# Kernel tuning notes

Measured on AMD Instinct MI355X. Metric: run time of the kernel, lower is better.

Reference implementation:

```python
import jax, jax.numpy as jnp
import numpy as np

N_NODES = 100000
N_GRAPHS = 512


def gcn_conv(x, W, b, src, dst, n_nodes):
    """PyG GCNConv: out = D^{-1/2} (A + I) D^{-1/2} (x W) + b, scatter at dst."""
    xw = x @ W  # [N, out_dim]
    # add self loops
    loop = jnp.arange(n_nodes, dtype=src.dtype)
    src_f = jnp.concatenate([src, loop])
    dst_f = jnp.concatenate([dst, loop])
    # symmetric normalization: deg from unit edge weights on dst
    deg = jax.ops.segment_sum(jnp.ones_like(dst_f, dtype=xw.dtype), dst_f,
                              num_segments=n_nodes)
    dinv = jnp.where(deg > 0, jax.lax.rsqrt(deg), 0.0)
    norm = dinv[src_f] * dinv[dst_f]  # [E+N]
    msg = xw[src_f] * norm[:, None]   # gather + scale, [E+N, out_dim]
    out = jax.ops.segment_sum(msg, dst_f, num_segments=n_nodes)
    return out + b


def global_mean_pool(x, batch, num_graphs):
    s = jax.ops.segment_sum(x, batch, num_segments=num_graphs)
    cnt = jax.ops.segment_sum(jnp.ones((x.shape[0],), x.dtype), batch,
                              num_segments=num_graphs)
    return s / jnp.maximum(cnt, 1.0)[:, None]


def setup_inputs() -> dict:
    key = jax.random.key(0)
    ks = jax.random.split(key, 10)
    d_in, h1, h2, d_out = 128, 128, 128, 32
    n_edges = 1600000
    x = jax.random.normal(ks[0], (N_NODES, d_in), dtype=jnp.float32)
    edge_index = jax.random.randint(ks[1], (2, n_edges), 0, N_NODES, dtype=jnp.int64)
    batch = jnp.sort(jax.random.randint(ks[2], (N_NODES,), 0, N_GRAPHS, dtype=jnp.int64))
    s1 = 1.0 / np.sqrt(d_in)
    s2 = 1.0 / np.sqrt(h1)
    s3 = 1.0 / np.sqrt(h2)
    W1 = jax.random.uniform(ks[3], (d_in, h1), jnp.float32, -s1, s1)
    b1 = jnp.zeros((h1,), jnp.float32)
    W2 = jax.random.uniform(ks[4], (h1, h2), jnp.float32, -s2, s2)
    b2 = jnp.zeros((h2,), jnp.float32)
    Wl = jax.random.uniform(ks[5], (h2, d_out), jnp.float32, -s3 * np.sqrt(6.0), s3 * np.sqrt(6.0))
    bl = jax.random.uniform(ks[6], (d_out,), jnp.float32, -s3, s3)
    return {"x": x, "edge_index": edge_index, "batch": batch,
            "W1": W1, "b1": b1, "W2": W2, "b2": b2, "Wl": Wl, "bl": bl}


def reference(x, edge_index, batch, W1, b1, W2, b2, Wl, bl):
    src, dst = edge_index[0], edge_index[1]
    h = gcn_conv(x, W1, b1, src, dst, N_NODES)
    h = jax.nn.relu(h)
    h = gcn_conv(h, W2, b2, src, dst, N_NODES)
    g = global_mean_pool(h, batch, N_GRAPHS)
    g = jax.nn.relu(g)
    return g @ Wl + bl
```

## Files before the change

### kernel.cpp

```cpp
#include <hip/hip_runtime.h>
#include <hip/hip_fp16.h>

#define DIM 128
#define NGRAPH 512
#define BUCKET_SHIFT 9
#define BUCKET_NODES 512

typedef _Float16 half8 __attribute__((ext_vector_type(8)));
typedef float floatx4 __attribute__((ext_vector_type(4)));

__device__ __forceinline__ int detect64(const int* __restrict__ ei) {
  int all0 = 1;
#pragma unroll
  for (int k = 0; k < 32; ++k) all0 &= (ei[2 * k + 1] == 0);
  return all0;
}

__device__ __forceinline__ int edge_at(const int* p, long long idx, int is64) {
  return is64 ? p[idx * 2] : p[(size_t)idx];
}

__global__ __launch_bounds__(256) void k_bucket_hist(const int* __restrict__ ei, int E,
                                                     int* __restrict__ bucket_count,
                                                     int nbuck) {
  __shared__ int h[256];
  int tid = threadIdx.x;
  h[tid] = 0;
  __syncthreads();
  int is64 = detect64(ei);
  int half = E >> 1;
  if (is64) {
    const int4* dp = (const int4*)(ei + 2 * (size_t)E);
    for (int t = blockIdx.x * 256 + tid; t < half; t += gridDim.x * 256) {
      int4 d = dp[t];
      atomicAdd(&h[d.x >> BUCKET_SHIFT], 1);
      atomicAdd(&h[d.z >> BUCKET_SHIFT], 1);
    }
  } else {
    const int2* dp = (const int2*)(ei + (size_t)E);
    for (int t = blockIdx.x * 256 + tid; t < half; t += gridDim.x * 256) {
      int2 d = dp[t];
      atomicAdd(&h[d.x >> BUCKET_SHIFT], 1);
      atomicAdd(&h[d.y >> BUCKET_SHIFT], 1);
    }
  }
  __syncthreads();
  if (tid < nbuck && h[tid]) atomicAdd(&bucket_count[tid], h[tid]);
  if ((E & 1) && blockIdx.x == 0 && tid == 0) {
    int d = edge_at(ei, (long long)E + (E - 1), is64);
    atomicAdd(&bucket_count[d >> BUCKET_SHIFT], 1);
  }
}

__global__ __launch_bounds__(256) void k_bucket_scan(const int* __restrict__ bucket_count,
                                                     int* __restrict__ bucket_off,
                                                     int* __restrict__ bucket_cursor,
                                                     int* __restrict__ row_off,
                                                     int nbuck, int N, int E) {
  __shared__ int s[256];
  int t = threadIdx.x;
  int v = (t < nbuck) ? bucket_count[t] : 0;
  s[t] = v;
  __syncthreads();
  for (int off = 1; off < 256; off <<= 1) {
    int u = (t >= off) ? s[t - off] : 0;
    __syncthreads();
    s[t] += u;
    __syncthreads();
  }
  int excl = s[t] - v;
  if (t < nbuck) { bucket_off[t] = excl; bucket_cursor[t] = excl; }
  if (t == 0) { bucket_off[nbuck] = E; row_off[N] = E; }
}

__global__ __launch_bounds__(256) void k_scatter(const int* __restrict__ ei, int E,
                                                 int* __restrict__ flag,
                                                 int* __restrict__ bucket_cursor,
                                                 int2* __restrict__ staging, int nbuck) {
  __shared__ int h[256];
  __shared__ int basebuf[256];
  int tid = threadIdx.x;
  int half = E >> 1;
  int ppb = (half + gridDim.x - 1) / gridDim.x;
  int lo = blockIdx.x * ppb;
  int hi = min(lo + ppb, half);
  h[tid] = 0;
  __syncthreads();
  int is64 = detect64(ei);
  if (blockIdx.x == 0 && tid == 0) *flag = is64;
  if (is64) {
    const int4* dp = (const int4*)(ei + 2 * (size_t)E);
    for (int t = lo + tid; t < hi; t += 256) {
      int4 d = dp[t];
      atomicAdd(&h[d.x >> BUCKET_SHIFT], 1);
      atomicAdd(&h[d.z >> BUCKET_SHIFT], 1);
    }
  } else {
    const int2* dp = (const int2*)(ei + (size_t)E);
    for (int t = lo + tid; t < hi; t += 256) {
      int2 d = dp[t];
      atomicAdd(&h[d.x >> BUCKET_SHIFT], 1);
      atomicAdd(&h[d.y >> BUCKET_SHIFT], 1);
    }
  }
  __syncthreads();
  if (tid < nbuck) {
    int c = h[tid];
    if (c) basebuf[tid] = atomicAdd(&bucket_cursor[tid], c);
    h[tid] = 0;
  }
  __syncthreads();
  if (is64) {
    const int4* sp = (const int4*)ei;
    const int4* dp = (const int4*)(ei + 2 * (size_t)E);
    for (int t = lo + tid; t < hi; t += 256) {
      int4 sv = sp[t];
      int4 dv = dp[t];
      int b0 = dv.x >> BUCKET_SHIFT;
      int l0 = atomicAdd(&h[b0], 1);
      staging[basebuf[b0] + l0] = make_int2(sv.x, dv.x);
      int b1 = dv.z >> BUCKET_SHIFT;
      int l1 = atomicAdd(&h[b1], 1);
      staging[basebuf[b1] + l1] = make_int2(sv.z, dv.z);
    }
  } else {
    const int2* sp = (const int2*)ei;
    const int2* dp = (const int2*)(ei + (size_t)E);
    for (int t = lo + tid; t < hi; t += 256) {
      int2 sv = sp[t];
      int2 dv = dp[t];
      int b0 = dv.x >> BUCKET_SHIFT;
      int l0 = atomicAdd(&h[b0], 1);
      staging[basebuf[b0] + l0] = make_int2(sv.x, dv.x);
      int b1 = dv.y >> BUCKET_SHIFT;
      int l1 = atomicAdd(&h[b1], 1);
      staging[basebuf[b1] + l1] = make_int2(sv.y, dv.y);
    }
  }
  if ((E & 1) && blockIdx.x == 0 && tid == 0) {
    int s0 = edge_at(ei, E - 1, is64);
    int d0 = edge_at(ei, (long long)E + (E - 1), is64);
    int pos = atomicAdd(&bucket_cursor[d0 >> BUCKET_SHIFT], 1);
    staging[pos] = make_int2(s0, d0);
  }
}

__global__ __launch_bounds__(256) void k_csr_build(const int2* __restrict__ staging,
                                                   const int* __restrict__ bucket_off,
                                                   int* __restrict__ row_off,
                                                   float* __restrict__ dinv,
                                                   int* __restrict__ csr_src, int N) {
  __shared__ int cnt_s[BUCKET_NODES];
  __shared__ int s[256];
  int tid = threadIdx.x;
  int b = blockIdx.x;
  int base = b << BUCKET_SHIFT;
  cnt_s[tid] = 0;
  cnt_s[tid + 256] = 0;
  __syncthreads();
  int start = bucket_off[b], end = bucket_off[b + 1];
  for (int i = start + tid; i < end; i += 256) {
    int2 e = staging[i];
    atomicAdd(&cnt_s[e.y - base], 1);
  }
  __syncthreads();
  int a0 = cnt_s[2 * tid], a1 = cnt_s[2 * tid + 1];
  int ps = a0 + a1;
  s[tid] = ps;
  __syncthreads();
  for (int off = 1; off < 256; off <<= 1) {
    int u = (tid >= off) ? s[tid - off] : 0;
    __syncthreads();
    s[tid] += u;
    __syncthreads();
  }
  int excl = s[tid] - ps;
  int r0 = start + excl;
  int r1 = r0 + a0;
  cnt_s[2 * tid] = r0;
  cnt_s[2 * tid + 1] = r1;
  int n0 = base + 2 * tid, n1 = n0 + 1;
  if (n0 < N) { row_off[n0] = r0; dinv[n0] = rsqrtf((float)(a0 + 1)); }
  if (n1 < N) { row_off[n1] = r1; dinv[n1] = rsqrtf((float)(a1 + 1)); }
  __syncthreads();
  for (int i = start + tid; i < end; i += 256) {
    int2 e = staging[i];
    int pos = atomicAdd(&cnt_s[e.y - base], 1);
    csr_src[pos] = e.x;
  }
}

template <int A16>
__global__ __launch_bounds__(256) void k_gemm_mfma(
    const void* __restrict__ Av, const float* __restrict__ W,
    const float* __restrict__ dinv, __half* __restrict__ Y, int M) {
  __shared__ _Float16 WH[16384];
  __shared__ _Float16 WL[16384];
  __shared__ _Float16 OT[4][16 * 128];
  int tid = threadIdx.x;

  for (int idx = tid; idx < 2048; idx += 256) {
    int l = idx & 63, c = (idx >> 6) & 7, s = idx >> 9;
    int kbase = s * 32 + ((l >> 4) << 3);
    int col = c * 16 + (l & 15);
#pragma unroll
    for (int j = 0; j < 8; ++j) {
      float w = W[(kbase + j) * 128 + col];
      _Float16 hh = (_Float16)w;
      WH[idx * 8 + j] = hh;
      WL[idx * 8 + j] = (_Float16)(w - (float)hh);
    }
  }
  __syncthreads();

  int wid = tid >> 6, l = tid & 63;
  int row0 = blockIdx.x * 64 + wid * 16;
  int arow = row0 + (l & 15);
  if (arow >= M) arow = M - 1;

  floatx4 acc[8];
#pragma unroll
  for (int c = 0; c < 8; ++c) acc[c] = (floatx4){0.f, 0.f, 0.f, 0.f};

#pragma unroll
  for (int s = 0; s < 4; ++s) {
    half8 ah, alo;
    if (A16) {
      const __half* A = (const __half*)Av;
      ah = *(const half8*)&A[(size_t)arow * 128 + s * 32 + ((l >> 4) << 3)];
    } else {
      const float* A = (const float*)Av;
      const float* ap = &A[(size_t)arow * 128 + s * 32 + ((l >> 4) << 3)];
      float4 f0 = *(const float4*)ap;
      float4 f1 = *(const float4*)(ap + 4);
      float fv[8] = {f0.x, f0.y, f0.z, f0.w, f1.x, f1.y, f1.z, f1.w};
#pragma unroll
      for (int j = 0; j < 8; ++j) {
        _Float16 hh = (_Float16)fv[j];
        ah[j] = hh;
        alo[j] = (_Float16)(fv[j] - (float)hh);
      }
    }
#pragma unroll
    for (int c = 0; c < 8; ++c) {
      int fi = ((s * 8 + c) * 64 + l) * 8;
      half8 bh = *(half8*)&WH[fi];
      half8 bl8 = *(half8*)&WL[fi];
      acc[c] = __builtin_amdgcn_mfma_f32_16x16x32_f16(ah, bh, acc[c], 0, 0, 0);
      if (!A16)
        acc[c] = __builtin_amdgcn_mfma_f32_16x16x32_f16(alo, bh, acc[c], 0, 0, 0);
      acc[c] = __builtin_amdgcn_mfma_f32_16x16x32_f16(ah, bl8, acc[c], 0, 0, 0);
    }
  }

  _Float16* ot = &OT[wid][0];
  int lrb = (l >> 4) * 4;
  float dv[4];
#pragma unroll
  for (int r = 0; r < 4; ++r) {
    int gr = row0 + lrb + r;
    dv[r] = (gr < M) ? dinv[gr] : 0.f;
  }
#pragma unroll
  for (int c = 0; c < 8; ++c)
#pragma unroll
    for (int r = 0; r < 4; ++r)
      ot[(lrb + r) * 128 + c * 16 + (l & 15)] = (_Float16)(acc[c][r] * dv[r]);
  const float4* otf = (const float4*)ot;
#pragma unroll
  for (int q = 0; q < 4; ++q) {
    int idx = q * 64 + l;
    int lrow = idx >> 4;
    int coff = (idx & 15) * 8;
    int grow = row0 + lrow;
    if (grow < M) *(float4*)&Y[(size_t)grow * 128 + coff] = otf[idx];
  }
}

__global__ __launch_bounds__(256) void k_aggregate(
    const __half* __restrict__ y, const int* __restrict__ csr_src,
    const int* __restrict__ row_off, const float* __restrict__ dinv,
    const float* __restrict__ bias, __half* __restrict__ out16, int do_relu, int N) {
  __shared__ int sidx[1024];
  int tid = threadIdx.x;
  int n0 = blockIdx.x * 4;
  int blockBeg = row_off[n0];
  int blockEnd = row_off[min(n0 + 4, N)];
  int len = blockEnd - blockBeg;
  bool staged = (len <= 1024);
  int nload = staged ? len : 0;
  for (int t = tid; t < nload; t += 256) sidx[t] = csr_src[blockBeg + t];
  __syncthreads();

  int wave = tid >> 6, l = tid & 63;
  int node = n0 + wave;
  if (node >= N) return;
  int g = l >> 4, q = l & 15;
  int beg = row_off[node], end = row_off[node + 1];

  float a0 = 0.f, a1 = 0.f, a2 = 0.f, a3 = 0.f, a4 = 0.f, a5 = 0.f, a6 = 0.f, a7 = 0.f;
#define ACC8(F4)                                                        \
  {                                                                     \
    float4 _f = (F4);                                                   \
    __half2 _h0 = *(__half2*)&_f.x, _h1 = *(__half2*)&_f.y;             \
    __half2 _h2 = *(__half2*)&_f.z, _h3 = *(__half2*)&_f.w;             \
    a0 += __low2float(_h0); a1 += __high2float(_h0);                    \
    a2 += __low2float(_h1); a3 += __high2float(_h1);                    \
    a4 += __low2float(_h2); a5 += __high2float(_h2);                    \
    a6 += __low2float(_h3); a7 += __high2float(_h3);                    \
  }
  if (g == 0) ACC8(*(const float4*)&y[(size_t)node * 128 + q * 8]);
  if (staged) {
    int rb = beg - blockBeg, re = end - blockBeg;
#pragma unroll 2
    for (int e = rb; e < re; e += 8) {
      int e0 = e + g, e1 = e + 4 + g;
      if (e0 < re) ACC8(*(const float4*)&y[(size_t)sidx[e0] * 128 + q * 8]);
      if (e1 < re) ACC8(*(const float4*)&y[(size_t)sidx[e1] * 128 + q * 8]);
    }
  } else {
    for (int e = beg; e < end; e += 8) {
      int e0 = e + g, e1 = e + 4 + g;
      if (e0 < end) ACC8(*(const float4*)&y[(size_t)csr_src[e0] * 128 + q * 8]);
      if (e1 < end) ACC8(*(const float4*)&y[(size_t)csr_src[e1] * 128 + q * 8]);
    }
  }
#undef ACC8
  a0 += __shfl_xor(a0, 16); a1 += __shfl_xor(a1, 16);
  a2 += __shfl_xor(a2, 16); a3 += __shfl_xor(a3, 16);
  a4 += __shfl_xor(a4, 16); a5 += __shfl_xor(a5, 16);
  a6 += __shfl_xor(a6, 16); a7 += __shfl_xor(a7, 16);
  a0 += __shfl_xor(a0, 32); a1 += __shfl_xor(a1, 32);
  a2 += __shfl_xor(a2, 32); a3 += __shfl_xor(a3, 32);
  a4 += __shfl_xor(a4, 32); a5 += __shfl_xor(a5, 32);
  a6 += __shfl_xor(a6, 32); a7 += __shfl_xor(a7, 32);

  if (g == 0) {
    float di = dinv[node];
    const float* bp = &bias[q * 8];
    float r0 = di * a0 + bp[0], r1 = di * a1 + bp[1];
    float r2 = di * a2 + bp[2], r3 = di * a3 + bp[3];
    float r4 = di * a4 + bp[4], r5 = di * a5 + bp[5];
    float r6 = di * a6 + bp[6], r7 = di * a7 + bp[7];
    if (do_relu) {
      r0 = fmaxf(r0, 0.f); r1 = fmaxf(r1, 0.f); r2 = fmaxf(r2, 0.f);
      r3 = fmaxf(r3, 0.f); r4 = fmaxf(r4, 0.f); r5 = fmaxf(r5, 0.f);
      r6 = fmaxf(r6, 0.f); r7 = fmaxf(r7, 0.f);
    }
    __half2 h[4];
    h[0] = __floats2half2_rn(r0, r1);
    h[1] = __floats2half2_rn(r2, r3);
    h[2] = __floats2half2_rn(r4, r5);
    h[3] = __floats2half2_rn(r6, r7);
    *(float4*)&out16[(size_t)node * 128 + q * 8] = *(float4*)h;
  }
}

__global__ __launch_bounds__(128) void k_pool_partial(
    const __half* __restrict__ h, const int* __restrict__ batch,
    float* __restrict__ pooled, int* __restrict__ pcnt, int n,
    const int* __restrict__ flag) {
  __shared__ int sbatch[128];
  int tid = threadIdx.x;
  int n0 = blockIdx.x * 128;
  int n1 = min(n0 + 128, n);
  int cnt = n1 - n0;
  int is64 = *flag;
  if (tid < cnt) sbatch[tid] = is64 ? batch[2 * (n0 + tid)] : batch[n0 + tid];
  __syncthreads();
  float acc = 0.f;
  int gcur = sbatch[0];
  int runlen = 0;
  for (int r = 0; r < cnt; ++r) {
    int g = sbatch[r];
    if (g != gcur) {
      atomicAdd(&pooled[(size_t)gcur * 128 + tid], acc);
      if (tid == 0) atomicAdd(&pcnt[gcur], runlen);
      acc = 0.f; runlen = 0; gcur = g;
    }
    acc += __half2float(h[(size_t)(n0 + r) * 128 + tid]);
    ++runlen;
  }
  atomicAdd(&pooled[(size_t)gcur * 128 + tid], acc);
  if (tid == 0) atomicAdd(&pcnt[gcur], runlen);
}

__global__ __launch_bounds__(256) void k_final2(
    const float* __restrict__ pooled, const int* __restrict__ pcnt,
    const float* __restrict__ Wl, const float* __restrict__ bl,
    float* __restrict__ out) {
  __shared__ float sW[128 * 32];
  __shared__ float sg[8][128];
  int tid = threadIdx.x;
  for (int t = tid; t < 128 * 32; t += 256) sW[t] = Wl[t];
  int r = blockIdx.x * 8 + (tid >> 5);
  int c = tid & 31;
  float inv = 1.f / fmaxf((float)pcnt[r], 1.f);
#pragma unroll
  for (int q = 0; q < 4; ++q)
    sg[tid >> 5][c * 4 + q] = fmaxf(pooled[(size_t)r * 128 + c * 4 + q] * inv, 0.f);
  __syncthreads();
  const float* g = sg[tid >> 5];
  float acc = bl[c];
#pragma unroll 8
  for (int k = 0; k < 128; ++k) acc += g[k] * sW[k * 32 + c];
  out[r * 32 + c] = acc;
}

extern "C" void kernel_launch(void* const* d_in, const int* in_sizes, int n_in,
                              void* d_out, int out_size, void* d_ws, size_t ws_size,
                              hipStream_t stream) {
  const float* x   = (const float*)d_in[0];
  const int* ei    = (const int*)d_in[1];
  const int* batch = (const int*)d_in[2];
  const float* W1  = (const float*)d_in[3];
  const float* b1  = (const float*)d_in[4];
  const float* W2  = (const float*)d_in[5];
  const float* b2  = (const float*)d_in[6];
  const float* Wl  = (const float*)d_in[7];
  const float* bl  = (const float*)d_in[8];
  float* out = (float*)d_out;

  const int N = in_sizes[0] / DIM;
  const int E = in_sizes[1] / 2;
  const int NBUCK = (N + BUCKET_NODES - 1) >> BUCKET_SHIFT;

  size_t need = (size_t)N * DIM * 2 + (size_t)N * DIM * 4 + (size_t)E * 4
              + (size_t)(N + 1) * 4 + (size_t)N * 4 + 3 * 1088 + 64
              + (size_t)NGRAPH * DIM * 4 + NGRAPH * 4;
  if (ws_size < need) return;

  char* w = (char*)d_ws;
  __half* bufY   = (__half*)w; w += (size_t)N * DIM * 2;
  __half* bufH16 = (__half*)w; w += (size_t)N * DIM * 4;
  int* csr_src  = (int*)w;    w += (size_t)E * 4;
  int* row_off  = (int*)w;    w += (size_t)(N + 1) * 4;
  float* dinv   = (float*)w;  w += (size_t)N * 4;
  int* bucket_count  = (int*)w; w += 1088;
  int* bucket_off    = (int*)w; w += 1088;
  int* bucket_cursor = (int*)w; w += 1088;
  int* flag     = (int*)w;    w += 64;
  float* pooled = (float*)w;  w += (size_t)NGRAPH * DIM * 4;
  int* pcnt     = (int*)w;    w += NGRAPH * 4;
  int2* staging = (int2*)bufY;

  hipMemsetAsync(bucket_count, 0, 1088, stream);
  hipMemsetAsync(pooled, 0, (size_t)NGRAPH * DIM * 4 + NGRAPH * 4, stream);
  k_bucket_hist<<<1024, 256, 0, stream>>>(ei, E, bucket_count, NBUCK);
  k_bucket_scan<<<1, 256, 0, stream>>>(bucket_count, bucket_off, bucket_cursor,
                                       row_off, NBUCK, N, E);
  k_scatter<<<1024, 256, 0, stream>>>(ei, E, flag, bucket_cursor, staging, NBUCK);
  k_csr_build<<<NBUCK, 256, 0, stream>>>(staging, bucket_off, row_off, dinv, csr_src, N);

  k_gemm_mfma<0><<<(N + 63) / 64, 256, 0, stream>>>(x, W1, dinv, bufY, N);
  k_aggregate<<<(N + 3) / 4, 256, 0, stream>>>(bufY, csr_src, row_off, dinv, b1,
                                               bufH16, 1, N);
  k_gemm_mfma<1><<<(N + 63) / 64, 256, 0, stream>>>(bufH16, W2, dinv, bufY, N);
  k_aggregate<<<(N + 3) / 4, 256, 0, stream>>>(bufY, csr_src, row_off, dinv, b2,
                                               bufH16, 0, N);
  k_pool_partial<<<(N + 127) / 128, 128, 0, stream>>>(bufH16, batch, pooled, pcnt, N, flag);
  k_final2<<<NGRAPH / 8, 256, 0, stream>>>(pooled, pcnt, Wl, bl, out);
}
```

Baseline: 427.3 us.

## Slice feature matrices into 16-column planes so aggregation gathers stay cache-resident

Y and H are now stored as 8 column slices of 16 halfs per node. The aggregation grid is split by slice, and each wave gathers 32-byte rows from one slice, so the gathered working set per slice (about 3.2 MB) can fit in L2/MALL instead of the full 25 MB matrix. The GEMM, pooling and aggregate kernels are all updated to the sliced layout. In exchange the node-level work is launched 8 times (CSR indices are reread 8 times), each gather fetches only 32 bytes, and the shared-memory index staging is removed.

```diff
diff --git a/kernel.cpp b/kernel.cpp
--- a/kernel.cpp
+++ b/kernel.cpp
@@ -227,7 +227,8 @@
     half8 ah, alo;
     if (A16) {
       const __half* A = (const __half*)Av;
-      ah = *(const half8*)&A[(size_t)arow * 128 + s * 32 + ((l >> 4) << 3)];
+      int q = s * 4 + (l >> 4);
+      ah = *(const half8*)&A[((size_t)(q >> 1) * M + arow) * 16 + (q & 1) * 8];
     } else {
       const float* A = (const float*)Av;
       const float* ap = &A[(size_t)arow * 128 + s * 32 + ((l >> 4) << 3)];
@@ -271,32 +272,26 @@
   for (int q = 0; q < 4; ++q) {
     int idx = q * 64 + l;
     int lrow = idx >> 4;
-    int coff = (idx & 15) * 8;
+    int q2 = idx & 15;
     int grow = row0 + lrow;
-    if (grow < M) *(float4*)&Y[(size_t)grow * 128 + coff] = otf[idx];
+    if (grow < M)
+      *(float4*)&Y[((size_t)(q2 >> 1) * M + grow) * 16 + (q2 & 1) * 8] = otf[idx];
   }
 }
 
 __global__ __launch_bounds__(256) void k_aggregate(
-    const __half* __restrict__ y, const int* __restrict__ csr_src,
+    const __half* __restrict__ Yb, const int* __restrict__ csr_src,
     const int* __restrict__ row_off, const float* __restrict__ dinv,
-    const float* __restrict__ bias, __half* __restrict__ out16, int do_relu, int N) {
-  __shared__ int sidx[1024];
-  int tid = threadIdx.x;
-  int n0 = blockIdx.x * 4;
-  int blockBeg = row_off[n0];
-  int blockEnd = row_off[min(n0 + 4, N)];
-  int len = blockEnd - blockBeg;
-  bool staged = (len <= 1024);
-  int nload = staged ? len : 0;
-  for (int t = tid; t < nload; t += 256) sidx[t] = csr_src[blockBeg + t];
-  __syncthreads();
-
-  int wave = tid >> 6, l = tid & 63;
-  int node = n0 + wave;
+    const float* __restrict__ bias, __half* __restrict__ outS, int do_relu, int N) {
+  int tid = threadIdx.x;
+  int slice = blockIdx.x & 7;
+  int chunk = blockIdx.x >> 3;
+  int node = chunk * 4 + (tid >> 6);
   if (node >= N) return;
-  int g = l >> 4, q = l & 15;
+  int l = tid & 63;
+  int j = l >> 1, half = l & 1;
   int beg = row_off[node], end = row_off[node + 1];
+  const __half* ybase = Yb + (size_t)slice * N * 16 + half * 8;
 
   float a0 = 0.f, a1 = 0.f, a2 = 0.f, a3 = 0.f, a4 = 0.f, a5 = 0.f, a6 = 0.f, a7 = 0.f;
 #define ACC8(F4)                                                        \
@@ -309,35 +304,23 @@
     a4 += __low2float(_h2); a5 += __high2float(_h2);                    \
     a6 += __low2float(_h3); a7 += __high2float(_h3);                    \
   }
-  if (g == 0) ACC8(*(const float4*)&y[(size_t)node * 128 + q * 8]);
-  if (staged) {
-    int rb = beg - blockBeg, re = end - blockBeg;
-#pragma unroll 2
-    for (int e = rb; e < re; e += 8) {
-      int e0 = e + g, e1 = e + 4 + g;
-      if (e0 < re) ACC8(*(const float4*)&y[(size_t)sidx[e0] * 128 + q * 8]);
-      if (e1 < re) ACC8(*(const float4*)&y[(size_t)sidx[e1] * 128 + q * 8]);
-    }
-  } else {
-    for (int e = beg; e < end; e += 8) {
-      int e0 = e + g, e1 = e + 4 + g;
-      if (e0 < end) ACC8(*(const float4*)&y[(size_t)csr_src[e0] * 128 + q * 8]);
-      if (e1 < end) ACC8(*(const float4*)&y[(size_t)csr_src[e1] * 128 + q * 8]);
-    }
+  if (j == 0) ACC8(*(const float4*)&ybase[(size_t)node * 16]);
+#pragma unroll 4
+  for (int e = beg + j; e < end; e += 32) {
+    int src = csr_src[e];
+    ACC8(*(const float4*)&ybase[(size_t)src * 16]);
   }
 #undef ACC8
-  a0 += __shfl_xor(a0, 16); a1 += __shfl_xor(a1, 16);
-  a2 += __shfl_xor(a2, 16); a3 += __shfl_xor(a3, 16);
-  a4 += __shfl_xor(a4, 16); a5 += __shfl_xor(a5, 16);
-  a6 += __shfl_xor(a6, 16); a7 += __shfl_xor(a7, 16);
-  a0 += __shfl_xor(a0, 32); a1 += __shfl_xor(a1, 32);
-  a2 += __shfl_xor(a2, 32); a3 += __shfl_xor(a3, 32);
-  a4 += __shfl_xor(a4, 32); a5 += __shfl_xor(a5, 32);
-  a6 += __shfl_xor(a6, 32); a7 += __shfl_xor(a7, 32);
-
-  if (g == 0) {
+#pragma unroll
+  for (int d = 2; d <= 32; d <<= 1) {
+    a0 += __shfl_xor(a0, d); a1 += __shfl_xor(a1, d);
+    a2 += __shfl_xor(a2, d); a3 += __shfl_xor(a3, d);
+    a4 += __shfl_xor(a4, d); a5 += __shfl_xor(a5, d);
+    a6 += __shfl_xor(a6, d); a7 += __shfl_xor(a7, d);
+  }
+  if (j == 0) {
     float di = dinv[node];
-    const float* bp = &bias[q * 8];
+    const float* bp = &bias[slice * 16 + half * 8];
     float r0 = di * a0 + bp[0], r1 = di * a1 + bp[1];
     float r2 = di * a2 + bp[2], r3 = di * a3 + bp[3];
     float r4 = di * a4 + bp[4], r5 = di * a5 + bp[5];
@@ -352,7 +335,7 @@
     h[1] = __floats2half2_rn(r2, r3);
     h[2] = __floats2half2_rn(r4, r5);
     h[3] = __floats2half2_rn(r6, r7);
-    *(float4*)&out16[(size_t)node * 128 + q * 8] = *(float4*)h;
+    *(float4*)&outS[((size_t)slice * N + node) * 16 + half * 8] = *(float4*)h;
   }
 }
 
@@ -368,6 +351,7 @@
   int is64 = *flag;
   if (tid < cnt) sbatch[tid] = is64 ? batch[2 * (n0 + tid)] : batch[n0 + tid];
   __syncthreads();
+  const __half* hcol = h + (size_t)(tid >> 4) * n * 16 + (tid & 15);
   float acc = 0.f;
   int gcur = sbatch[0];
   int runlen = 0;
@@ -378,7 +362,7 @@
       if (tid == 0) atomicAdd(&pcnt[gcur], runlen);
       acc = 0.f; runlen = 0; gcur = g;
     }
-    acc += __half2float(h[(size_t)(n0 + r) * 128 + tid]);
+    acc += __half2float(hcol[(size_t)(n0 + r) * 16]);
     ++runlen;
   }
   atomicAdd(&pooled[(size_t)gcur * 128 + tid], acc);
@@ -397,8 +381,10 @@
   int c = tid & 31;
   float inv = 1.f / fmaxf((float)pcnt[r], 1.f);
 #pragma unroll
-  for (int q = 0; q < 4; ++q)
-    sg[tid >> 5][c * 4 + q] = fmaxf(pooled[(size_t)r * 128 + c * 4 + q] * inv, 0.f);
+  for (int q = 0; q < 4; ++q) {
+    int t = c * 4 + q;
+    sg[tid >> 5][t] = fmaxf(pooled[(size_t)r * 128 + t] * inv, 0.f);
+  }
   __syncthreads();
   const float* g = sg[tid >> 5];
   float acc = bl[c];
@@ -452,12 +438,13 @@
   k_scatter<<<1024, 256, 0, stream>>>(ei, E, flag, bucket_cursor, staging, NBUCK);
   k_csr_build<<<NBUCK, 256, 0, stream>>>(staging, bucket_off, row_off, dinv, csr_src, N);
 
+  int aggGrid = ((N + 3) / 4) * 8;
   k_gemm_mfma<0><<<(N + 63) / 64, 256, 0, stream>>>(x, W1, dinv, bufY, N);
-  k_aggregate<<<(N + 3) / 4, 256, 0, stream>>>(bufY, csr_src, row_off, dinv, b1,
-                                               bufH16, 1, N);
+  k_aggregate<<<aggGrid, 256, 0, stream>>>(bufY, csr_src, row_off, dinv, b1,
+                                           bufH16, 1, N);
   k_gemm_mfma<1><<<(N + 63) / 64, 256, 0, stream>>>(bufH16, W2, dinv, bufY, N);
-  k_aggregate<<<(N + 3) / 4, 256, 0, stream>>>(bufY, csr_src, row_off, dinv, b2,
-                                               bufH16, 0, N);
+  k_aggregate<<<aggGrid, 256, 0, stream>>>(bufY, csr_src, row_off, dinv, b2,
+                                           bufH16, 0, N);
   k_pool_partial<<<(N + 127) / 128, 128, 0, stream>>>(bufH16, batch, pooled, pcnt, N, flag);
   k_final2<<<NGRAPH / 8, 256, 0, stream>>>(pooled, pcnt, Wl, bl, out);
 }
```

Result: slower. 929.8 us (+117.6%).
